# Optimization experiments

Measured on AMD Instinct MI355X. Metric: run time of the kernel, lower is better.

The kernel has to match this reference:

```python
import jax, jax.numpy as jnp
import numpy as np
from jax import lax

B, C, H, W = 16, 256, 64, 64
K = 3  # kernel_size


def setup_inputs() -> dict:
    key = jax.random.key(0)
    k1, k2, k3, k4 = jax.random.split(key, 4)
    x = jax.random.normal(k1, (B, C, H, W), dtype=jnp.float32)
    # nn.Parameter init is ones; perturb so softmax is non-trivial
    dir_weight_h = jnp.ones((1, C, 1, 1), jnp.float32) + 0.1 * jax.random.normal(k2, (1, C, 1, 1), jnp.float32)
    dir_weight_w = jnp.ones((1, C, 1, 1), jnp.float32) + 0.1 * jax.random.normal(k3, (1, C, 1, 1), jnp.float32)
    gate_w = 0.1 * jax.random.normal(k4, (), jnp.float32)  # 1x1 conv on 1 channel = scalar
    gate_b = jnp.float32(-1.0)  # init.constant_(gate.bias, -1.0)
    return {"x": x, "dir_weight_h": dir_weight_h, "dir_weight_w": dir_weight_w,
            "gate_w": gate_w, "gate_b": gate_b}


def reference(x, dir_weight_h, dir_weight_w, gate_w, gate_b):
    b, c, h, w = x.shape
    # directional softmax-weighted global pooling
    ww = jax.nn.softmax(dir_weight_w, axis=1)            # (1,C,1,1)
    global_h = jnp.mean(x * ww, axis=3, keepdims=True)   # (B,C,H,1)
    wh = jax.nn.softmax(dir_weight_h, axis=1)
    global_w = jnp.mean(x * wh, axis=2, keepdims=True)   # (B,C,1,W)
    global_dir = global_h + global_w                     # broadcast -> (B,C,H,W)

    # local covariance: unfold(x1)*unfold(x2) mean over k*k taps
    # == KxK box-sum of (x1*x2) with zero padding, divided by k*k
    half = c // 2
    prod = x[:, :half] * x[:, half:]                     # (B,C/2,H,W)
    cov = lax.reduce_window(prod, 0.0, lax.add,
                            window_dimensions=(1, 1, K, K),
                            window_strides=(1, 1, 1, 1),
                            padding=[(0, 0), (0, 0), (K // 2, K // 2), (K // 2, K // 2)]) / (K * K)

    consistency = jnp.mean(jnp.abs(cov), axis=1, keepdims=True)  # (B,1,H,W)
    local_anomaly = 1.0 - jnp.clip(consistency, 0.0, 1.0)

    fusion = jnp.mean(global_dir, axis=1, keepdims=True) * local_anomaly  # (B,1,H,W)
    attention = jax.nn.sigmoid(gate_w * fusion + gate_b)  # 1x1 conv with scalar weight/bias
    return x * attention
```

## Files before the change

### kernel.cpp

```cpp
#include <hip/hip_runtime.h>
#include <math.h>

#define NB 16
#define NC 256
#define NH 64
#define NW 64
#define HALF 128
#define PLANE (NH*NW)
#define NPG 32

#define WS_ATT 0

#define SCR_CONS 0
#define SCR_GHP  2097152
#define SCR_GWP  (2097152 + 32768)

#define HPAD 76

__device__ __forceinline__ float sum4(float4 v) { return (v.x+v.y)+(v.z+v.w); }

__device__ __forceinline__ float4 hsum4(float4 p, int fc) {
    float pl = __shfl_up(p.w, 1);
    float pr = __shfl_down(p.x, 1);
    if (fc == 0)  pl = 0.f;
    if (fc == 15) pr = 0.f;
    float4 h;
    h.x = pl  + p.x + p.y;
    h.y = p.x + p.y + p.z;
    h.z = p.y + p.z + p.w;
    h.w = p.z + p.w + pr;
    return h;
}

__global__ __launch_bounds__(256) void k_reduce(const float* __restrict__ x,
                                                const float* __restrict__ dwh,
                                                const float* __restrict__ dww,
                                                float* __restrict__ scr) {
    __shared__ float ew[256], eh[256];
    __shared__ float wsum[8];
    __shared__ float hs[64*HPAD];

    const int t   = threadIdx.x;
    const int v   = t >> 6;
    const int lane= t & 63;
    const int g16 = t >> 4;
    const int w4  = t & 15;

    const int blk = blockIdx.x;
    const int pg  = blk & (NPG-1);
    const int b   = blk >> 5;

    {
        const float vw = dww[t], vh = dwh[t];
        const float evw = expf(vw), evh = expf(vh);
        ew[t] = evw; eh[t] = evh;
        float sw = evw, sh = evh;
        #pragma unroll
        for (int m = 1; m < 64; m <<= 1) { sw += __shfl_xor(sw, m); sh += __shfl_xor(sh, m); }
        if (lane == 0) { wsum[v] = sw; wsum[4+v] = sh; }
    }
    __syncthreads();
    const float invSw = 1.f/((wsum[0]+wsum[1])+(wsum[2]+wsum[3]));
    const float invSh = 1.f/((wsum[4]+wsum[5])+(wsum[6]+wsum[7]));

    float4 c4a0 = {0,0,0,0}, c4a1 = {0,0,0,0}, c4a2 = {0,0,0,0}, c4a3 = {0,0,0,0};
    float  gh0 = 0.f, gh1 = 0.f, gh2 = 0.f, gh3 = 0.f;
    float4 colacc = {0,0,0,0};
    float4* hsf4 = reinterpret_cast<float4*>(hs);

    #pragma unroll
    for (int pp = 0; pp < 4; ++pp) {
        const int c1 = pg*4 + pp;
        const float ww1 = ew[c1]*invSw, ww2 = ew[c1+HALF]*invSw;
        const float wh1 = eh[c1]*invSh, wh2 = eh[c1+HALF]*invSh;

        const float4* q1 = reinterpret_cast<const float4*>(x + ((size_t)(b*NC + c1))*PLANE);
        const float4* q2 = reinterpret_cast<const float4*>(x + ((size_t)(b*NC + c1 + HALF))*PLANE);

        const float4 a0 = q1[t], a1 = q1[t+256], a2 = q1[t+512], a3 = q1[t+768];
        const float4 b0 = q2[t], b1 = q2[t+256], b2 = q2[t+512], b3 = q2[t+768];

        gh0 += ww1*sum4(a0) + ww2*sum4(b0);
        gh1 += ww1*sum4(a1) + ww2*sum4(b1);
        gh2 += ww1*sum4(a2) + ww2*sum4(b2);
        gh3 += ww1*sum4(a3) + ww2*sum4(b3);
        colacc.x += wh1*((a0.x+a1.x)+(a2.x+a3.x)) + wh2*((b0.x+b1.x)+(b2.x+b3.x));
        colacc.y += wh1*((a0.y+a1.y)+(a2.y+a3.y)) + wh2*((b0.y+b1.y)+(b2.y+b3.y));
        colacc.z += wh1*((a0.z+a1.z)+(a2.z+a3.z)) + wh2*((b0.z+b1.z)+(b2.z+b3.z));
        colacc.w += wh1*((a0.w+a1.w)+(a2.w+a3.w)) + wh2*((b0.w+b1.w)+(b2.w+b3.w));

        float4 p, h;
        p.x=a0.x*b0.x; p.y=a0.y*b0.y; p.z=a0.z*b0.z; p.w=a0.w*b0.w;
        h = hsum4(p, w4); hsf4[(g16 +  0)*19 + w4] = h;
        p.x=a1.x*b1.x; p.y=a1.y*b1.y; p.z=a1.z*b1.z; p.w=a1.w*b1.w;
        h = hsum4(p, w4); hsf4[(g16 + 16)*19 + w4] = h;
        p.x=a2.x*b2.x; p.y=a2.y*b2.y; p.z=a2.z*b2.z; p.w=a2.w*b2.w;
        h = hsum4(p, w4); hsf4[(g16 + 32)*19 + w4] = h;
        p.x=a3.x*b3.x; p.y=a3.y*b3.y; p.z=a3.z*b3.z; p.w=a3.w*b3.w;
        h = hsum4(p, w4); hsf4[(g16 + 48)*19 + w4] = h;

        __syncthreads();

        {
            const int r = g16;
            const float4 mid = hsf4[r*19 + w4];
            float4 top = {0,0,0,0}, bot;
            if (r > 0) top = hsf4[(r-1)*19 + w4];
            bot = hsf4[(r+1)*19 + w4];
            c4a0.x += fabsf(top.x+mid.x+bot.x); c4a0.y += fabsf(top.y+mid.y+bot.y);
            c4a0.z += fabsf(top.z+mid.z+bot.z); c4a0.w += fabsf(top.w+mid.w+bot.w);
        }
        {
            const int r = g16 + 16;
            const float4 mid = hsf4[r*19 + w4];
            const float4 top = hsf4[(r-1)*19 + w4];
            const float4 bot = hsf4[(r+1)*19 + w4];
            c4a1.x += fabsf(top.x+mid.x+bot.x); c4a1.y += fabsf(top.y+mid.y+bot.y);
            c4a1.z += fabsf(top.z+mid.z+bot.z); c4a1.w += fabsf(top.w+mid.w+bot.w);
        }
        {
            const int r = g16 + 32;
            const float4 mid = hsf4[r*19 + w4];
            const float4 top = hsf4[(r-1)*19 + w4];
            const float4 bot = hsf4[(r+1)*19 + w4];
            c4a2.x += fabsf(top.x+mid.x+bot.x); c4a2.y += fabsf(top.y+mid.y+bot.y);
            c4a2.z += fabsf(top.z+mid.z+bot.z); c4a2.w += fabsf(top.w+mid.w+bot.w);
        }
        {
            const int r = g16 + 48;
            const float4 mid = hsf4[r*19 + w4];
            const float4 top = hsf4[(r-1)*19 + w4];
            float4 bot = {0,0,0,0};
            if (r < 63) bot = hsf4[(r+1)*19 + w4];
            c4a3.x += fabsf(top.x+mid.x+bot.x); c4a3.y += fabsf(top.y+mid.y+bot.y);
            c4a3.z += fabsf(top.z+mid.z+bot.z); c4a3.w += fabsf(top.w+mid.w+bot.w);
        }

        __syncthreads();
    }

    const float SC  = 1.0f/(9.0f*128.0f);
    const float GSC = 1.0f/16384.0f;

    {
        float4* dst = reinterpret_cast<float4*>(scr) + ((size_t)pg << 14) + (b << 10);
        float4 s;
        s.x=c4a0.x*SC; s.y=c4a0.y*SC; s.z=c4a0.z*SC; s.w=c4a0.w*SC; dst[(g16+ 0)*16 + w4] = s;
        s.x=c4a1.x*SC; s.y=c4a1.y*SC; s.z=c4a1.z*SC; s.w=c4a1.w*SC; dst[(g16+16)*16 + w4] = s;
        s.x=c4a2.x*SC; s.y=c4a2.y*SC; s.z=c4a2.z*SC; s.w=c4a2.w*SC; dst[(g16+32)*16 + w4] = s;
        s.x=c4a3.x*SC; s.y=c4a3.y*SC; s.z=c4a3.z*SC; s.w=c4a3.w*SC; dst[(g16+48)*16 + w4] = s;
    }

    {
        float* ghdst = scr + SCR_GHP + (size_t)(b*NPG + pg)*64;
        float g;
        g = gh0; g += __shfl_xor(g,1); g += __shfl_xor(g,2); g += __shfl_xor(g,4); g += __shfl_xor(g,8);
        if (w4 == 0) ghdst[g16 +  0] = g * GSC;
        g = gh1; g += __shfl_xor(g,1); g += __shfl_xor(g,2); g += __shfl_xor(g,4); g += __shfl_xor(g,8);
        if (w4 == 0) ghdst[g16 + 16] = g * GSC;
        g = gh2; g += __shfl_xor(g,1); g += __shfl_xor(g,2); g += __shfl_xor(g,4); g += __shfl_xor(g,8);
        if (w4 == 0) ghdst[g16 + 32] = g * GSC;
        g = gh3; g += __shfl_xor(g,1); g += __shfl_xor(g,2); g += __shfl_xor(g,4); g += __shfl_xor(g,8);
        if (w4 == 0) ghdst[g16 + 48] = g * GSC;
    }

    hsf4[t] = colacc;
    __syncthreads();
    if (t < 16) {
        float4 s = {0,0,0,0};
        #pragma unroll
        for (int g = 0; g < 16; ++g) {
            const float4 vv = hsf4[g*16 + t];
            s.x += vv.x; s.y += vv.y; s.z += vv.z; s.w += vv.w;
        }
        s.x *= GSC; s.y *= GSC; s.z *= GSC; s.w *= GSC;
        *reinterpret_cast<float4*>(scr + SCR_GWP + (size_t)(b*NPG + pg)*64 + t*4) = s;
    }
}

__global__ __launch_bounds__(256) void k_att(float* __restrict__ ws,
                                             const float* __restrict__ scr,
                                             const float* __restrict__ pgw,
                                             const float* __restrict__ pgb) {
    __shared__ __align__(16) float sgw[64];
    __shared__ __align__(16) float sgh[4];
    const int t = threadIdx.x;
    const int s = blockIdx.x & 15;
    const int b = blockIdx.x >> 4;

    if (t < 64) {
        float acc = 0.f;
        #pragma unroll 8
        for (int pg = 0; pg < NPG; ++pg)
            acc += scr[SCR_GWP + (size_t)(b*NPG + pg)*64 + t];
        sgw[t] = acc;
    } else if (t < 68) {
        const int r = s*4 + (t - 64);
        float acc = 0.f;
        #pragma unroll 8
        for (int pg = 0; pg < NPG; ++pg)
            acc += scr[SCR_GHP + (size_t)(b*NPG + pg)*64 + r];
        sgh[t-64] = acc;
    }
    __syncthreads();

    if (t < 64) {
        const int u = (b << 10) + (s << 6) + t;
        const float4* cp = reinterpret_cast<const float4*>(scr);
        float4 sm = {0.f,0.f,0.f,0.f};
        #pragma unroll
        for (int g = 0; g < NPG; ++g) {
            const float4 vv = cp[((size_t)g << 14) + u];
            sm.x += vv.x; sm.y += vv.y; sm.z += vv.z; sm.w += vv.w;
        }
        const float ghv  = sgh[t >> 4];
        const float4 gwv = *reinterpret_cast<const float4*>(&sgw[(t & 15)*4]);
        const float gW = pgw[0], gB = pgb[0];

        float4 o;
        float z;
        z = gW*(ghv+gwv.x)*(1.f - fminf(fmaxf(sm.x,0.f),1.f)) + gB; o.x = 1.f/(1.f+expf(-z));
        z = gW*(ghv+gwv.y)*(1.f - fminf(fmaxf(sm.y,0.f),1.f)) + gB; o.y = 1.f/(1.f+expf(-z));
        z = gW*(ghv+gwv.z)*(1.f - fminf(fmaxf(sm.z,0.f),1.f)) + gB; o.z = 1.f/(1.f+expf(-z));
        z = gW*(ghv+gwv.w)*(1.f - fminf(fmaxf(sm.w,0.f),1.f)) + gB; o.w = 1.f/(1.f+expf(-z));
        reinterpret_cast<float4*>(ws + WS_ATT)[u] = o;
    }
}

__global__ __launch_bounds__(256) void k_apply(const float* __restrict__ x,
                                               const float* __restrict__ ws,
                                               float* __restrict__ out) {
    const float* att = ws + WS_ATT;
    const int total4 = NB*NC*NH*NW/4;
    const int stride = gridDim.x * blockDim.x;
    for (int i = blockIdx.x*blockDim.x + threadIdx.x; i < total4; i += stride) {
        const int w4 = i & 15;
        const int h  = (i >> 4) & 63;
        const int b  = i >> 18;
        const float4 xv = reinterpret_cast<const float4*>(x)[i];
        const float4 av = reinterpret_cast<const float4*>(att)[(b << 10) + (h << 4) + w4];
        float4 o;
        o.x = xv.x*av.x; o.y = xv.y*av.y; o.z = xv.z*av.z; o.w = xv.w*av.w;
        reinterpret_cast<float4*>(out)[i] = o;
    }
}

extern "C" void kernel_launch(void* const* d_in, const int* in_sizes, int n_in,
                              void* d_out, int out_size, void* d_ws, size_t ws_size,
                              hipStream_t stream) {
    const float* x   = (const float*)d_in[0];
    const float* dwh = (const float*)d_in[1];
    const float* dww = (const float*)d_in[2];
    const float* pgw = (const float*)d_in[3];
    const float* pgb = (const float*)d_in[4];
    float* out = (float*)d_out;
    float* ws  = (float*)d_ws;
    float* scr = out;

    k_reduce<<<NB*NPG, 256, 0, stream>>>(x, dwh, dww, scr);
    k_att<<<256, 256, 0, stream>>>(ws, scr, pgw, pgb);
    k_apply<<<2048, 256, 0, stream>>>(x, ws, out);
}
```

Measured before the change: 50.43 us.

## Double reduce-kernel block count and spread partial-sum reduction across all threads

Splits the channel-pair work across 64 groups instead of 32, so each reduce block handles 2 channel pairs instead of 4 and twice as many blocks run. The per-group partial layout for the global row and column sums is transposed so the attention kernel reads each row with contiguous float4 loads. The attention kernel now uses all 256 threads to sum the 64 covariance partials in four slices before a shared-memory combine. The cost is twice the scratch writes and reads for the partial covariance maps, and less work per block over which to spread the softmax setup.

```diff
diff --git a/kernel.cpp b/kernel.cpp
--- a/kernel.cpp
+++ b/kernel.cpp
@@ -7,15 +7,13 @@
 #define NW 64
 #define HALF 128
 #define PLANE (NH*NW)
-#define NPG 32
+#define NPG 64
 
 #define WS_ATT 0
 
 #define SCR_CONS 0
-#define SCR_GHP  2097152
-#define SCR_GWP  (2097152 + 32768)
-
-#define HPAD 76
+#define SCR_GHP  4194304
+#define SCR_GWP  (4194304 + 65536)
 
 __device__ __forceinline__ float sum4(float4 v) { return (v.x+v.y)+(v.z+v.w); }
 
@@ -38,7 +36,7 @@
                                                 float* __restrict__ scr) {
     __shared__ float ew[256], eh[256];
     __shared__ float wsum[8];
-    __shared__ float hs[64*HPAD];
+    __shared__ float hs[64*76];
 
     const int t   = threadIdx.x;
     const int v   = t >> 6;
@@ -48,7 +46,7 @@
 
     const int blk = blockIdx.x;
     const int pg  = blk & (NPG-1);
-    const int b   = blk >> 5;
+    const int b   = blk >> 6;
 
     {
         const float vw = dww[t], vh = dwh[t];
@@ -68,9 +66,9 @@
     float4 colacc = {0,0,0,0};
     float4* hsf4 = reinterpret_cast<float4*>(hs);
 
-    #pragma unroll
-    for (int pp = 0; pp < 4; ++pp) {
-        const int c1 = pg*4 + pp;
+    #pragma unroll 1
+    for (int pp = 0; pp < 2; ++pp) {
+        const int c1 = pg*2 + pp;
         const float ww1 = ew[c1]*invSw, ww2 = ew[c1+HALF]*invSw;
         const float wh1 = eh[c1]*invSh, wh2 = eh[c1+HALF]*invSh;
 
@@ -101,39 +99,18 @@
 
         __syncthreads();
 
-        {
-            const int r = g16;
+        #pragma unroll
+        for (int k = 0; k < 4; ++k) {
+            const int r = g16 + 16*k;
             const float4 mid = hsf4[r*19 + w4];
-            float4 top = {0,0,0,0}, bot;
-            if (r > 0) top = hsf4[(r-1)*19 + w4];
-            bot = hsf4[(r+1)*19 + w4];
-            c4a0.x += fabsf(top.x+mid.x+bot.x); c4a0.y += fabsf(top.y+mid.y+bot.y);
-            c4a0.z += fabsf(top.z+mid.z+bot.z); c4a0.w += fabsf(top.w+mid.w+bot.w);
-        }
-        {
-            const int r = g16 + 16;
-            const float4 mid = hsf4[r*19 + w4];
-            const float4 top = hsf4[(r-1)*19 + w4];
-            const float4 bot = hsf4[(r+1)*19 + w4];
-            c4a1.x += fabsf(top.x+mid.x+bot.x); c4a1.y += fabsf(top.y+mid.y+bot.y);
-            c4a1.z += fabsf(top.z+mid.z+bot.z); c4a1.w += fabsf(top.w+mid.w+bot.w);
-        }
-        {
-            const int r = g16 + 32;
-            const float4 mid = hsf4[r*19 + w4];
-            const float4 top = hsf4[(r-1)*19 + w4];
-            const float4 bot = hsf4[(r+1)*19 + w4];
-            c4a2.x += fabsf(top.x+mid.x+bot.x); c4a2.y += fabsf(top.y+mid.y+bot.y);
-            c4a2.z += fabsf(top.z+mid.z+bot.z); c4a2.w += fabsf(top.w+mid.w+bot.w);
-        }
-        {
-            const int r = g16 + 48;
-            const float4 mid = hsf4[r*19 + w4];
-            const float4 top = hsf4[(r-1)*19 + w4];
-            float4 bot = {0,0,0,0};
+            float4 top = {0,0,0,0}, bot = {0,0,0,0};
+            if (r > 0)  top = hsf4[(r-1)*19 + w4];
             if (r < 63) bot = hsf4[(r+1)*19 + w4];
-            c4a3.x += fabsf(top.x+mid.x+bot.x); c4a3.y += fabsf(top.y+mid.y+bot.y);
-            c4a3.z += fabsf(top.z+mid.z+bot.z); c4a3.w += fabsf(top.w+mid.w+bot.w);
+            float4* acc = (k == 0) ? &c4a0 : (k == 1) ? &c4a1 : (k == 2) ? &c4a2 : &c4a3;
+            acc->x += fabsf(top.x+mid.x+bot.x);
+            acc->y += fabsf(top.y+mid.y+bot.y);
+            acc->z += fabsf(top.z+mid.z+bot.z);
+            acc->w += fabsf(top.w+mid.w+bot.w);
         }
 
         __syncthreads();
@@ -152,29 +129,24 @@
     }
 
     {
-        float* ghdst = scr + SCR_GHP + (size_t)(b*NPG + pg)*64;
         float g;
         g = gh0; g += __shfl_xor(g,1); g += __shfl_xor(g,2); g += __shfl_xor(g,4); g += __shfl_xor(g,8);
-        if (w4 == 0) ghdst[g16 +  0] = g * GSC;
+        if (w4 == 0) scr[SCR_GHP + (size_t)(b*NH + g16 +  0)*64 + pg] = g * GSC;
         g = gh1; g += __shfl_xor(g,1); g += __shfl_xor(g,2); g += __shfl_xor(g,4); g += __shfl_xor(g,8);
-        if (w4 == 0) ghdst[g16 + 16] = g * GSC;
+        if (w4 == 0) scr[SCR_GHP + (size_t)(b*NH + g16 + 16)*64 + pg] = g * GSC;
         g = gh2; g += __shfl_xor(g,1); g += __shfl_xor(g,2); g += __shfl_xor(g,4); g += __shfl_xor(g,8);
-        if (w4 == 0) ghdst[g16 + 32] = g * GSC;
+        if (w4 == 0) scr[SCR_GHP + (size_t)(b*NH + g16 + 32)*64 + pg] = g * GSC;
         g = gh3; g += __shfl_xor(g,1); g += __shfl_xor(g,2); g += __shfl_xor(g,4); g += __shfl_xor(g,8);
-        if (w4 == 0) ghdst[g16 + 48] = g * GSC;
+        if (w4 == 0) scr[SCR_GHP + (size_t)(b*NH + g16 + 48)*64 + pg] = g * GSC;
     }
 
     hsf4[t] = colacc;
     __syncthreads();
-    if (t < 16) {
-        float4 s = {0,0,0,0};
-        #pragma unroll
-        for (int g = 0; g < 16; ++g) {
-            const float4 vv = hsf4[g*16 + t];
-            s.x += vv.x; s.y += vv.y; s.z += vv.z; s.w += vv.w;
-        }
-        s.x *= GSC; s.y *= GSC; s.z *= GSC; s.w *= GSC;
-        *reinterpret_cast<float4*>(scr + SCR_GWP + (size_t)(b*NPG + pg)*64 + t*4) = s;
+    if (t < 64) {
+        float s = 0.f;
+        #pragma unroll
+        for (int g = 0; g < 16; ++g) s += hs[g*64 + t];
+        scr[SCR_GWP + (size_t)(b*NW + t)*64 + pg] = s * GSC;
     }
 }
 
@@ -182,37 +154,50 @@
                                              const float* __restrict__ scr,
                                              const float* __restrict__ pgw,
                                              const float* __restrict__ pgb) {
+    __shared__ __align__(16) float4 sacc[4][64];
     __shared__ __align__(16) float sgw[64];
     __shared__ __align__(16) float sgh[4];
     const int t = threadIdx.x;
     const int s = blockIdx.x & 15;
     const int b = blockIdx.x >> 4;
-
+    const int px = t & 63;
+    const int q  = t >> 6;
+
+    {
+        const int u = (b << 10) + (s << 6) + px;
+        const float4* cp = reinterpret_cast<const float4*>(scr);
+        float4 sm = {0.f,0.f,0.f,0.f};
+        #pragma unroll
+        for (int g = 0; g < 16; ++g) {
+            const float4 vv = cp[((size_t)(q*16 + g) << 14) + u];
+            sm.x += vv.x; sm.y += vv.y; sm.z += vv.z; sm.w += vv.w;
+        }
+        sacc[q][px] = sm;
+    }
     if (t < 64) {
+        const float4* gp = reinterpret_cast<const float4*>(scr + SCR_GWP + (size_t)(b*NW + t)*64);
         float acc = 0.f;
-        #pragma unroll 8
-        for (int pg = 0; pg < NPG; ++pg)
-            acc += scr[SCR_GWP + (size_t)(b*NPG + pg)*64 + t];
+        #pragma unroll
+        for (int i = 0; i < 16; ++i) acc += sum4(gp[i]);
         sgw[t] = acc;
     } else if (t < 68) {
         const int r = s*4 + (t - 64);
+        const float4* gp = reinterpret_cast<const float4*>(scr + SCR_GHP + (size_t)(b*NH + r)*64);
         float acc = 0.f;
-        #pragma unroll 8
-        for (int pg = 0; pg < NPG; ++pg)
-            acc += scr[SCR_GHP + (size_t)(b*NPG + pg)*64 + r];
+        #pragma unroll
+        for (int i = 0; i < 16; ++i) acc += sum4(gp[i]);
         sgh[t-64] = acc;
     }
     __syncthreads();
 
     if (t < 64) {
+        const float4 s0 = sacc[0][t], s1 = sacc[1][t], s2 = sacc[2][t], s3 = sacc[3][t];
+        float4 sm;
+        sm.x = (s0.x+s1.x)+(s2.x+s3.x);
+        sm.y = (s0.y+s1.y)+(s2.y+s3.y);
+        sm.z = (s0.z+s1.z)+(s2.z+s3.z);
+        sm.w = (s0.w+s1.w)+(s2.w+s3.w);
         const int u = (b << 10) + (s << 6) + t;
-        const float4* cp = reinterpret_cast<const float4*>(scr);
-        float4 sm = {0.f,0.f,0.f,0.f};
-        #pragma unroll
-        for (int g = 0; g < NPG; ++g) {
-            const float4 vv = cp[((size_t)g << 14) + u];
-            sm.x += vv.x; sm.y += vv.y; sm.z += vv.z; sm.w += vv.w;
-        }
         const float ghv  = sgh[t >> 4];
         const float4 gwv = *reinterpret_cast<const float4*>(&sgw[(t & 15)*4]);
         const float gW = pgw[0], gB = pgb[0];
```

Result: faster. 48.90 us (-3.0%).
